# Kernel tuning notes

Measured on AMD Instinct MI355X. Metric: run time of the kernel, lower is better.

Reference implementation:

```python
import jax, jax.numpy as jnp
import numpy as np


def setup_inputs() -> dict:
    key = jax.random.key(0)
    k1, k2, k3 = jax.random.split(key, 3)
    B, L, D = 4, 2056, 1024  # L = K + T = 8 + 2048
    x = jax.random.normal(k1, (B, L, D), dtype=jnp.float32)
    # Linear weights stored as (in_features, out_features); no bias (config.bias=False)
    W_attn = jax.random.normal(k2, (D, 3 * D), dtype=jnp.float32) * 0.02
    W_proj = jax.random.normal(k3, (D, D), dtype=jnp.float32) * 0.02
    return {"x": x, "W_attn": W_attn, "W_proj": W_proj, "n_head": 16, "n_memory": 8}


def reference(x, W_attn, W_proj, n_head, n_memory):
    B, L, C = x.shape
    K = n_memory
    T = L - K
    hd = C // n_head
    scale = 1.0 / np.sqrt(hd).astype(np.float32)

    qkv = x @ W_attn                      # (B, L, 3C)
    q, k, v = jnp.split(qkv, 3, axis=2)
    # (B, H, L, hd)
    q = q.reshape(B, L, n_head, hd).transpose(0, 2, 1, 3)
    k = k.reshape(B, L, n_head, hd).transpose(0, 2, 1, 3)
    v = v.reshape(B, L, n_head, hd).transpose(0, 2, 1, 3)

    att = jnp.einsum("bhqd,bhkd->bhqk", q, k) * scale  # (B, H, L, L)

    # Mask: all-True except the (seq x seq) block which is causal (lower-tri).
    # Memory rows (first K) attend everywhere; seq rows attend to all memory + causal seq.
    mask = jnp.ones((L, L), dtype=bool)
    seq_causal = jnp.tril(jnp.ones((T, T), dtype=bool))
    mask = mask.at[K:, K:].set(seq_causal)

    att = jnp.where(mask[None, None, :, :], att, jnp.float32(-jnp.inf))
    att = jax.nn.softmax(att, axis=-1)

    y = jnp.einsum("bhqk,bhkd->bhqd", att, v)  # (B, H, L, hd)
    y = y.transpose(0, 2, 1, 3).reshape(B, L, C)
    return y @ W_proj
```

## Files before the change

### kernel.cpp

```cpp
#include <hip/hip_runtime.h>
#include <hip/hip_bf16.h>
#include <hip/hip_fp16.h>

typedef _Float16 f16x8 __attribute__((ext_vector_type(8)));
typedef _Float16 f16x4 __attribute__((ext_vector_type(4)));
typedef float f32x4 __attribute__((ext_vector_type(4)));

typedef const __attribute__((address_space(1))) void gvoid_t;
typedef __attribute__((address_space(3))) void svoid_t;

constexpr int Bb = 4, Lq = 2056, Dd = 1024, NH = 16, HD = 64, NMEM = 8;
constexpr int Mtot = Bb * Lq;
constexpr int KEYS = 64;
constexpr int NT = (Lq + KEYS - 1) / KEYS;
constexpr int NTQP = 17;
constexpr int LqV = 2064;

__device__ inline float fexp2(float x) {
  float r;
  asm("v_exp_f32 %0, %1" : "=v"(r) : "v"(x));
  return r;
}

__global__ __launch_bounds__(256) void cast_f16(const float* __restrict__ in,
                                                _Float16* __restrict__ out, int n8) {
  int i = blockIdx.x * blockDim.x + threadIdx.x;
  if (i >= n8) return;
  const float4* p = reinterpret_cast<const float4*>(in) + (size_t)i * 2;
  float4 a = p[0], b = p[1];
  f16x8 o;
  o[0] = (_Float16)a.x; o[1] = (_Float16)a.y; o[2] = (_Float16)a.z; o[3] = (_Float16)a.w;
  o[4] = (_Float16)b.x; o[5] = (_Float16)b.y; o[6] = (_Float16)b.z; o[7] = (_Float16)b.w;
  *(reinterpret_cast<f16x8*>(out) + i) = o;
}

__global__ void transpose_cast(const float* __restrict__ in, _Float16* __restrict__ out,
                               int rows, int cols) {
  __shared__ float t[32][33];
  int c0 = blockIdx.x * 32, r0 = blockIdx.y * 32;
  int tx = threadIdx.x, ty = threadIdx.y;
#pragma unroll
  for (int i = 0; i < 4; ++i)
    t[ty + i * 8][tx] = in[(size_t)(r0 + ty + i * 8) * cols + c0 + tx];
  __syncthreads();
#pragma unroll
  for (int i = 0; i < 4; ++i)
    out[(size_t)(c0 + ty + i * 8) * rows + r0 + tx] = (_Float16)t[tx][ty + i * 8];
}

template <int EPI>
__global__ __launch_bounds__(256) void gemm_f16(
    const _Float16* __restrict__ A, const _Float16* __restrict__ Bt,
    int M, int N, int Kd, float* __restrict__ Cf,
    _Float16* __restrict__ qout, _Float16* __restrict__ kout, _Float16* __restrict__ vtout) {
  constexpr int BM = 128, BN = 128, BK = 64;
  __shared__ _Float16 smem[2][2 * BM * BK];
  const int tid = threadIdx.x;
  const int wid = tid >> 6, lane = tid & 63;
  const int wr = wid >> 1, wc = wid & 1;
  const int l16 = lane & 15, lq = lane >> 4;

  const int gx = gridDim.x;
  const int nwg = gx * gridDim.y;
  const int i0 = blockIdx.y * gx + blockIdx.x;
  const int cpx = nwg >> 3;
  const int logical = (i0 & 7) * cpx + (i0 >> 3);
  const int m0 = (logical / gx) * BM, n0 = (logical % gx) * BN;

  f32x4 acc[4][4];
#pragma unroll
  for (int i = 0; i < 4; ++i)
#pragma unroll
    for (int j = 0; j < 4; ++j) acc[i][j] = (f32x4){0.f, 0.f, 0.f, 0.f};

  auto stage = [&](int sb, int kt) {
    const size_t kbase = (size_t)kt * BK;
    _Float16* sm = smem[sb];
#pragma unroll
    for (int c = 0; c < 4; ++c) {
      int q = wid * 256 + c * 64 + lane;
      int r = q >> 3, cc = q & 7;
      int gr = m0 + r; gr = gr < M ? gr : M - 1;
      const _Float16* src = A + (size_t)gr * Kd + kbase + ((cc ^ (r & 7)) << 3);
      __builtin_amdgcn_global_load_lds((gvoid_t*)src,
          (svoid_t*)(sm + (size_t)(wid * 256 + c * 64) * 8), 16, 0, 0);
    }
#pragma unroll
    for (int c = 0; c < 4; ++c) {
      int q = wid * 256 + c * 64 + lane;
      int r = q >> 3, cc = q & 7;
      const _Float16* src = Bt + (size_t)(n0 + r) * Kd + kbase + ((cc ^ (r & 7)) << 3);
      __builtin_amdgcn_global_load_lds((gvoid_t*)src,
          (svoid_t*)(sm + BM * BK + (size_t)(wid * 256 + c * 64) * 8), 16, 0, 0);
    }
  };

  const int KT = Kd / BK;
  stage(0, 0);
  __syncthreads();
  int sbuf = 0;
  for (int kt = 0; kt < KT; ++kt) {
    if (kt + 1 < KT) stage(sbuf ^ 1, kt + 1);
    const _Float16* sm = smem[sbuf];
#pragma unroll
    for (int kk = 0; kk < 2; ++kk) {
      f16x8 af[4], bfr[4];
#pragma unroll
      for (int i = 0; i < 4; ++i) {
        int r = wr * 64 + i * 16 + l16;
        int off = r * 64 + (((kk * 4 + lq) ^ (r & 7)) << 3);
        af[i] = *(const f16x8*)(sm + off);
      }
#pragma unroll
      for (int j = 0; j < 4; ++j) {
        int r = wc * 64 + j * 16 + l16;
        int off = BM * BK + r * 64 + (((kk * 4 + lq) ^ (r & 7)) << 3);
        bfr[j] = *(const f16x8*)(sm + off);
      }
#pragma unroll
      for (int i = 0; i < 4; ++i)
#pragma unroll
        for (int j = 0; j < 4; ++j)
          acc[i][j] = __builtin_amdgcn_mfma_f32_16x16x32_f16(af[i], bfr[j], acc[i][j], 0, 0, 0);
    }
    __syncthreads();
    sbuf ^= 1;
  }

  if (EPI == 1 && n0 >= 2 * Dd) {
#pragma unroll
    for (int i = 0; i < 4; ++i) {
      int mb = m0 + wr * 64 + i * 16 + lq * 4;
      if (mb >= M) continue;
      int b = mb / Lq, l = mb - b * Lq;
#pragma unroll
      for (int j = 0; j < 4; ++j) {
        int n = n0 + wc * 64 + j * 16 + l16;
        int h = (n >> 6) & 15, d = n & 63;
        if (l + 4 <= Lq) {
          int kk = l & 63;
          int ks = kk >> 5, rem = kk & 31, half = rem >> 4, idx = rem & 15;
          int col = (l & ~63) + (ks * 4 + (idx >> 2)) * 8 + half * 4;
          f16x4 pk;
          pk[0] = (_Float16)acc[i][j][0]; pk[1] = (_Float16)acc[i][j][1];
          pk[2] = (_Float16)acc[i][j][2]; pk[3] = (_Float16)acc[i][j][3];
          *(f16x4*)(vtout + ((size_t)(b * NH + h) * HD + d) * LqV + col) = pk;
        } else {
#pragma unroll
          for (int r = 0; r < 4; ++r) {
            int m = mb + r;
            if (m >= M) continue;
            int b2 = m / Lq, l2 = m - b2 * Lq;
            int kk = l2 & 63;
            int ks = kk >> 5, rem = kk & 31, half = rem >> 4, idx = rem & 15;
            int col = (l2 & ~63) + (ks * 4 + (idx >> 2)) * 8 + half * 4 + (idx & 3);
            vtout[((size_t)(b2 * NH + h) * HD + d) * LqV + col] = (_Float16)acc[i][j][r];
          }
        }
      }
    }
  } else {
#pragma unroll
    for (int i = 0; i < 4; ++i) {
#pragma unroll
      for (int r = 0; r < 4; ++r) {
        int m = m0 + wr * 64 + i * 16 + lq * 4 + r;
        if (m >= M) continue;
        if (EPI == 0) {
#pragma unroll
          for (int j = 0; j < 4; ++j) {
            int n = n0 + wc * 64 + j * 16 + l16;
            Cf[(size_t)m * N + n] = acc[i][j][r];
          }
        } else {
          int b = m / Lq, l = m - b * Lq;
#pragma unroll
          for (int j = 0; j < 4; ++j) {
            int n = n0 + wc * 64 + j * 16 + l16;
            int which = n >> 10, h = (n >> 6) & 15, d = n & 63;
            int bh = b * NH + h;
            _Float16 v = (_Float16)acc[i][j][r];
            if (which == 0)
              qout[((size_t)bh * Lq + l) * HD + d] = v;
            else
              kout[((size_t)bh * Lq + l) * HD + d] = v;
          }
        }
      }
    }
  }
}

__global__ __launch_bounds__(256) void attn_f16(const _Float16* __restrict__ qm,
                                                const _Float16* __restrict__ km,
                                                const _Float16* __restrict__ vt,
                                                _Float16* __restrict__ y) {
  __shared__ _Float16 kls[2][KEYS * HD];
  __shared__ _Float16 vls[2][KEYS * HD];

  const int i0 = blockIdx.y * (int)gridDim.x + blockIdx.x;
  const int logical = (i0 & 7) * (NTQP * Bb * NH / 8) + (i0 >> 3);
  const int bh = logical / NTQP;
  const int px = logical % NTQP;

  const int wid = threadIdx.x >> 6, lane = threadIdx.x & 63;
  const int l16 = lane & 15, lq = lane >> 4;

  const _Float16* qbase = qm + (size_t)bh * Lq * HD;
  const _Float16* kbase = km + (size_t)bh * Lq * HD;
  const _Float16* vbase = vt + (size_t)bh * HD * LqV;
  const int b = bh >> 4, h = bh & 15;

  const _Float16 QSC = (_Float16)(0.125f * 1.44269504f);

  f16x8 ones;
#pragma unroll
  for (int e = 0; e < 8; ++e) ones[e] = (_Float16)1.0f;

  const int qA = (wid * 2 + 0) * 64 + lane, qB = (wid * 2 + 1) * 64 + lane;
  const int rA = qA >> 3, cA = qA & 7;
  const int rB = qB >> 3, cB = qB & 7;
  const int ofA = (cA ^ (rA & 7)) << 3;
  const int ofB = (cB ^ (rB & 7)) << 3;
  _Float16* dKA0 = &kls[0][(wid * 2 + 0) * 512]; _Float16* dKB0 = &kls[0][(wid * 2 + 1) * 512];
  _Float16* dKA1 = &kls[1][(wid * 2 + 0) * 512]; _Float16* dKB1 = &kls[1][(wid * 2 + 1) * 512];
  _Float16* dVA0 = &vls[0][(wid * 2 + 0) * 512]; _Float16* dVB0 = &vls[0][(wid * 2 + 1) * 512];
  _Float16* dVA1 = &vls[1][(wid * 2 + 0) * 512]; _Float16* dVB1 = &vls[1][(wid * 2 + 1) * 512];

  const int nseg = (px == 0) ? 1 : 2;
  for (int seg = 0; seg < nseg; ++seg) {
    const int qt = (px == 0) ? 0 : (seg == 0 ? NT - px : px);
    const int qr0 = qt * 64 + wid * 16;

    int qrow = qr0 + l16; if (qrow > Lq - 1) qrow = Lq - 1;
    f16x8 qf0 = *(const f16x8*)(qbase + (size_t)qrow * HD + lq * 8);
    f16x8 qf1 = *(const f16x8*)(qbase + (size_t)qrow * HD + 32 + lq * 8);
#pragma unroll
    for (int e = 0; e < 8; ++e) {
      qf0[e] *= QSC;
      qf1[e] *= QSC;
    }

    const int irow = qr0 + l16;
    const int kmax = (irow < NMEM) ? (Lq - 1) : (irow < Lq - 1 ? irow : Lq - 1);

    f32x4 o[4];
#pragma unroll
    for (int dt = 0; dt < 4; ++dt) o[dt] = (f32x4){0.f, 0.f, 0.f, 0.f};
    f32x4 ol = (f32x4){0.f, 0.f, 0.f, 0.f};

    const int ntiles = (qt == 0) ? NT : (qt + 1 < NT ? qt + 1 : NT);

    const _Float16* pkA = kbase + (size_t)rA * HD + ofA;
    const _Float16* pkB = kbase + (size_t)rB * HD + ofB;
    const _Float16* pvA = vbase + (size_t)rA * LqV + ofA;
    const _Float16* pvB = vbase + (size_t)rB * LqV + ofB;

    auto stage_fast = [&](_Float16* dK0, _Float16* dK1, _Float16* dV0, _Float16* dV1) {
      __builtin_amdgcn_global_load_lds((gvoid_t*)pkA, (svoid_t*)dK0, 16, 0, 0);
      __builtin_amdgcn_global_load_lds((gvoid_t*)pkB, (svoid_t*)dK1, 16, 0, 0);
      __builtin_amdgcn_global_load_lds((gvoid_t*)pvA, (svoid_t*)dV0, 16, 0, 0);
      __builtin_amdgcn_global_load_lds((gvoid_t*)pvB, (svoid_t*)dV1, 16, 0, 0);
      pkA += KEYS * HD; pkB += KEYS * HD; pvA += KEYS; pvB += KEYS;
    };
    auto stage_clamp = [&](_Float16* dK0, _Float16* dK1, _Float16* dV0, _Float16* dV1) {
      int keyA = 2048 + rA; if (keyA > Lq - 1) keyA = Lq - 1;
      int keyB = 2048 + rB; if (keyB > Lq - 1) keyB = Lq - 1;
      __builtin_amdgcn_global_load_lds((gvoid_t*)(kbase + (size_t)keyA * HD + ofA),
                                       (svoid_t*)dK0, 16, 0, 0);
      __builtin_amdgcn_global_load_lds((gvoid_t*)(kbase + (size_t)keyB * HD + ofB),
                                       (svoid_t*)dK1, 16, 0, 0);
      int kcA = 2048 + ofA; if (kcA + 8 > LqV) kcA = LqV - 8;
      int kcB = 2048 + ofB; if (kcB + 8 > LqV) kcB = LqV - 8;
      __builtin_amdgcn_global_load_lds((gvoid_t*)(vbase + (size_t)rA * LqV + kcA),
                                       (svoid_t*)dV0, 16, 0, 0);
      __builtin_amdgcn_global_load_lds((gvoid_t*)(vbase + (size_t)rB * LqV + kcB),
                                       (svoid_t*)dV1, 16, 0, 0);
    };

    auto compute = [&](const _Float16* Kl, const _Float16* Vl, int t) {
      const int j0 = t * KEYS;
      const bool fastw = ((t + 1) * KEYS <= qr0);
      const int lim = kmax - j0;
#pragma unroll
      for (int ks = 0; ks < 2; ++ks) {
        const int r0 = ks * 32 + l16, r1 = r0 + 16;
        f16x8 ka0 = *(const f16x8*)(Kl + r0 * 64 + ((lq ^ (r0 & 7)) << 3));
        f16x8 kb0 = *(const f16x8*)(Kl + r0 * 64 + (((4 + lq) ^ (r0 & 7)) << 3));
        f16x8 ka1 = *(const f16x8*)(Kl + r1 * 64 + ((lq ^ (r1 & 7)) << 3));
        f16x8 kb1 = *(const f16x8*)(Kl + r1 * 64 + (((4 + lq) ^ (r1 & 7)) << 3));
        f32x4 s0 = (f32x4){0.f, 0.f, 0.f, 0.f};
        f32x4 s1 = (f32x4){0.f, 0.f, 0.f, 0.f};
        __builtin_amdgcn_s_setprio(1);
        s0 = __builtin_amdgcn_mfma_f32_16x16x32_f16(ka0, qf0, s0, 0, 0, 0);
        s0 = __builtin_amdgcn_mfma_f32_16x16x32_f16(kb0, qf1, s0, 0, 0, 0);
        s1 = __builtin_amdgcn_mfma_f32_16x16x32_f16(ka1, qf0, s1, 0, 0, 0);
        s1 = __builtin_amdgcn_mfma_f32_16x16x32_f16(kb1, qf1, s1, 0, 0, 0);
        __builtin_amdgcn_s_setprio(0);

        f16x8 pf;
        if (fastw) {
#pragma unroll
          for (int r = 0; r < 4; ++r) {
            pf[r] = (_Float16)fexp2(s0[r]);
            pf[4 + r] = (_Float16)fexp2(s1[r]);
          }
        } else {
          const int kb = ks * 32 + lq * 4;
#pragma unroll
          for (int r = 0; r < 4; ++r) {
            pf[r] = (kb + r <= lim) ? (_Float16)fexp2(s0[r]) : (_Float16)0.f;
            pf[4 + r] = (kb + 16 + r <= lim) ? (_Float16)fexp2(s1[r]) : (_Float16)0.f;
          }
        }

        __builtin_amdgcn_s_setprio(1);
        ol = __builtin_amdgcn_mfma_f32_16x16x32_f16(pf, ones, ol, 0, 0, 0);
#pragma unroll
        for (int dt = 0; dt < 4; ++dt) {
          const int vr = dt * 16 + l16;
          const int g = ks * 4 + lq;
          f16x8 vf = *(const f16x8*)(Vl + vr * 64 + ((g ^ (vr & 7)) << 3));
          o[dt] = __builtin_amdgcn_mfma_f32_16x16x32_f16(pf, vf, o[dt], 0, 0, 0);
        }
        __builtin_amdgcn_s_setprio(0);
      }
    };

    stage_fast(dKA0, dKB0, dVA0, dVB0);
    __syncthreads();
    int t = 0;
    for (;;) {
      {
        int nxt = t + 1;
        if (nxt < ntiles) {
          if (nxt == NT - 1) stage_clamp(dKA1, dKB1, dVA1, dVB1);
          else stage_fast(dKA1, dKB1, dVA1, dVB1);
        }
      }
      compute(kls[0], vls[0], t);
      __syncthreads();
      if (++t >= ntiles) break;
      {
        int nxt = t + 1;
        if (nxt < ntiles) {
          if (nxt == NT - 1) stage_clamp(dKA0, dKB0, dVA0, dVB0);
          else stage_fast(dKA0, dKB0, dVA0, dVB0);
        }
      }
      compute(kls[1], vls[1], t);
      __syncthreads();
      if (++t >= ntiles) break;
    }

#pragma unroll
    for (int r = 0; r < 4; ++r) {
      int orow = qr0 + lq * 4 + r;
      if (orow >= Lq) continue;
      float inv = 1.0f / ol[r];
#pragma unroll
      for (int dt = 0; dt < 4; ++dt)
        y[((size_t)(b * Lq + orow)) * Dd + h * HD + dt * 16 + l16] = (_Float16)(o[dt][r] * inv);
    }
  }
}

extern "C" void kernel_launch(void* const* d_in, const int* in_sizes, int n_in,
                              void* d_out, int out_size, void* d_ws, size_t ws_size,
                              hipStream_t stream) {
  (void)in_sizes; (void)n_in; (void)out_size; (void)ws_size;
  const float* x = (const float*)d_in[0];
  const float* W_attn = (const float*)d_in[1];
  const float* W_proj = (const float*)d_in[2];
  float* out = (float*)d_out;

  char* w = (char*)d_ws;
  _Float16* xh  = (_Float16*)(w);
  _Float16* wta = (_Float16*)(w + 16842752);
  _Float16* wtp = (_Float16*)(w + 23134208);
  _Float16* qh  = (_Float16*)(w + 25231360);
  _Float16* kh  = (_Float16*)(w + 42074112);
  _Float16* vth = (_Float16*)(w + 58916864);
  _Float16* yh  = xh;

  cast_f16<<<dim3((Mtot * Dd) / 8 / 256), dim3(256), 0, stream>>>(x, xh, (Mtot * Dd) / 8);
  transpose_cast<<<dim3(3 * Dd / 32, Dd / 32), dim3(32, 8), 0, stream>>>(W_attn, wta, Dd, 3 * Dd);
  transpose_cast<<<dim3(Dd / 32, Dd / 32), dim3(32, 8), 0, stream>>>(W_proj, wtp, Dd, Dd);

  gemm_f16<1><<<dim3(3 * Dd / 128, (Mtot + 127) / 128), dim3(256), 0, stream>>>(
      xh, wta, Mtot, 3 * Dd, Dd, nullptr, qh, kh, vth);

  attn_f16<<<dim3(NTQP, Bb * NH), dim3(256), 0, stream>>>(qh, kh, vth, yh);

  gemm_f16<0><<<dim3(Dd / 128, (Mtot + 127) / 128), dim3(256), 0, stream>>>(
      yh, wtp, Mtot, Dd, Dd, out, nullptr, nullptr, nullptr);
}
```

Before: 204.7 us.

## Process both paired query tiles in one pass sharing staged K/V tiles

```diff
diff --git a/kernel.cpp b/kernel.cpp
--- a/kernel.cpp
+++ b/kernel.cpp
@@ -217,9 +217,41 @@
 #pragma unroll
   for (int e = 0; e < 8; ++e) ones[e] = (_Float16)1.0f;
 
-  const int qA = (wid * 2 + 0) * 64 + lane, qB = (wid * 2 + 1) * 64 + lane;
-  const int rA = qA >> 3, cA = qA & 7;
-  const int rB = qB >> 3, cB = qB & 7;
+  const int qtA = (px == 0) ? 0 : NT - px;
+  const int ntA = (px == 0) ? NT : (qtA + 1 < NT ? qtA + 1 : NT);
+  const int ntB = (px == 0) ? 0 : px + 1;
+  const int qr0A = qtA * 64 + wid * 16;
+  const int qr0B = px * 64 + wid * 16;
+
+  int qrowA = qr0A + l16; if (qrowA > Lq - 1) qrowA = Lq - 1;
+  f16x8 qfA0 = *(const f16x8*)(qbase + (size_t)qrowA * HD + lq * 8);
+  f16x8 qfA1 = *(const f16x8*)(qbase + (size_t)qrowA * HD + 32 + lq * 8);
+  int qrowB = qr0B + l16;
+  f16x8 qfB0 = *(const f16x8*)(qbase + (size_t)qrowB * HD + lq * 8);
+  f16x8 qfB1 = *(const f16x8*)(qbase + (size_t)qrowB * HD + 32 + lq * 8);
+#pragma unroll
+  for (int e = 0; e < 8; ++e) {
+    qfA0[e] *= QSC; qfA1[e] *= QSC;
+    qfB0[e] *= QSC; qfB1[e] *= QSC;
+  }
+
+  const int irowA = qr0A + l16;
+  const int kmaxA = (irowA < NMEM) ? (Lq - 1) : (irowA < Lq - 1 ? irowA : Lq - 1);
+  const int irowB = qr0B + l16;
+  const int kmaxB = (irowB < NMEM) ? (Lq - 1) : irowB;
+
+  f32x4 oA[4], oB[4];
+#pragma unroll
+  for (int dt = 0; dt < 4; ++dt) {
+    oA[dt] = (f32x4){0.f, 0.f, 0.f, 0.f};
+    oB[dt] = (f32x4){0.f, 0.f, 0.f, 0.f};
+  }
+  f32x4 olA = (f32x4){0.f, 0.f, 0.f, 0.f};
+  f32x4 olB = (f32x4){0.f, 0.f, 0.f, 0.f};
+
+  const int qA_ = (wid * 2 + 0) * 64 + lane, qB_ = (wid * 2 + 1) * 64 + lane;
+  const int rA = qA_ >> 3, cA = qA_ & 7;
+  const int rB = qB_ >> 3, cB = qB_ & 7;
   const int ofA = (cA ^ (rA & 7)) << 3;
   const int ofB = (cB ^ (rB & 7)) << 3;
   _Float16* dKA0 = &kls[0][(wid * 2 + 0) * 512]; _Float16* dKB0 = &kls[0][(wid * 2 + 1) * 512];
@@ -227,140 +259,154 @@
   _Float16* dVA0 = &vls[0][(wid * 2 + 0) * 512]; _Float16* dVB0 = &vls[0][(wid * 2 + 1) * 512];
   _Float16* dVA1 = &vls[1][(wid * 2 + 0) * 512]; _Float16* dVB1 = &vls[1][(wid * 2 + 1) * 512];
 
-  const int nseg = (px == 0) ? 1 : 2;
-  for (int seg = 0; seg < nseg; ++seg) {
-    const int qt = (px == 0) ? 0 : (seg == 0 ? NT - px : px);
-    const int qr0 = qt * 64 + wid * 16;
-
-    int qrow = qr0 + l16; if (qrow > Lq - 1) qrow = Lq - 1;
-    f16x8 qf0 = *(const f16x8*)(qbase + (size_t)qrow * HD + lq * 8);
-    f16x8 qf1 = *(const f16x8*)(qbase + (size_t)qrow * HD + 32 + lq * 8);
-#pragma unroll
-    for (int e = 0; e < 8; ++e) {
-      qf0[e] *= QSC;
-      qf1[e] *= QSC;
-    }
-
-    const int irow = qr0 + l16;
-    const int kmax = (irow < NMEM) ? (Lq - 1) : (irow < Lq - 1 ? irow : Lq - 1);
-
-    f32x4 o[4];
-#pragma unroll
-    for (int dt = 0; dt < 4; ++dt) o[dt] = (f32x4){0.f, 0.f, 0.f, 0.f};
-    f32x4 ol = (f32x4){0.f, 0.f, 0.f, 0.f};
-
-    const int ntiles = (qt == 0) ? NT : (qt + 1 < NT ? qt + 1 : NT);
-
-    const _Float16* pkA = kbase + (size_t)rA * HD + ofA;
-    const _Float16* pkB = kbase + (size_t)rB * HD + ofB;
-    const _Float16* pvA = vbase + (size_t)rA * LqV + ofA;
-    const _Float16* pvB = vbase + (size_t)rB * LqV + ofB;
-
-    auto stage_fast = [&](_Float16* dK0, _Float16* dK1, _Float16* dV0, _Float16* dV1) {
-      __builtin_amdgcn_global_load_lds((gvoid_t*)pkA, (svoid_t*)dK0, 16, 0, 0);
-      __builtin_amdgcn_global_load_lds((gvoid_t*)pkB, (svoid_t*)dK1, 16, 0, 0);
-      __builtin_amdgcn_global_load_lds((gvoid_t*)pvA, (svoid_t*)dV0, 16, 0, 0);
-      __builtin_amdgcn_global_load_lds((gvoid_t*)pvB, (svoid_t*)dV1, 16, 0, 0);
-      pkA += KEYS * HD; pkB += KEYS * HD; pvA += KEYS; pvB += KEYS;
-    };
-    auto stage_clamp = [&](_Float16* dK0, _Float16* dK1, _Float16* dV0, _Float16* dV1) {
-      int keyA = 2048 + rA; if (keyA > Lq - 1) keyA = Lq - 1;
-      int keyB = 2048 + rB; if (keyB > Lq - 1) keyB = Lq - 1;
-      __builtin_amdgcn_global_load_lds((gvoid_t*)(kbase + (size_t)keyA * HD + ofA),
-                                       (svoid_t*)dK0, 16, 0, 0);
-      __builtin_amdgcn_global_load_lds((gvoid_t*)(kbase + (size_t)keyB * HD + ofB),
-                                       (svoid_t*)dK1, 16, 0, 0);
-      int kcA = 2048 + ofA; if (kcA + 8 > LqV) kcA = LqV - 8;
-      int kcB = 2048 + ofB; if (kcB + 8 > LqV) kcB = LqV - 8;
-      __builtin_amdgcn_global_load_lds((gvoid_t*)(vbase + (size_t)rA * LqV + kcA),
-                                       (svoid_t*)dV0, 16, 0, 0);
-      __builtin_amdgcn_global_load_lds((gvoid_t*)(vbase + (size_t)rB * LqV + kcB),
-                                       (svoid_t*)dV1, 16, 0, 0);
-    };
-
-    auto compute = [&](const _Float16* Kl, const _Float16* Vl, int t) {
-      const int j0 = t * KEYS;
-      const bool fastw = ((t + 1) * KEYS <= qr0);
-      const int lim = kmax - j0;
-#pragma unroll
-      for (int ks = 0; ks < 2; ++ks) {
-        const int r0 = ks * 32 + l16, r1 = r0 + 16;
-        f16x8 ka0 = *(const f16x8*)(Kl + r0 * 64 + ((lq ^ (r0 & 7)) << 3));
-        f16x8 kb0 = *(const f16x8*)(Kl + r0 * 64 + (((4 + lq) ^ (r0 & 7)) << 3));
-        f16x8 ka1 = *(const f16x8*)(Kl + r1 * 64 + ((lq ^ (r1 & 7)) << 3));
-        f16x8 kb1 = *(const f16x8*)(Kl + r1 * 64 + (((4 + lq) ^ (r1 & 7)) << 3));
-        f32x4 s0 = (f32x4){0.f, 0.f, 0.f, 0.f};
-        f32x4 s1 = (f32x4){0.f, 0.f, 0.f, 0.f};
-        __builtin_amdgcn_s_setprio(1);
-        s0 = __builtin_amdgcn_mfma_f32_16x16x32_f16(ka0, qf0, s0, 0, 0, 0);
-        s0 = __builtin_amdgcn_mfma_f32_16x16x32_f16(kb0, qf1, s0, 0, 0, 0);
-        s1 = __builtin_amdgcn_mfma_f32_16x16x32_f16(ka1, qf0, s1, 0, 0, 0);
-        s1 = __builtin_amdgcn_mfma_f32_16x16x32_f16(kb1, qf1, s1, 0, 0, 0);
-        __builtin_amdgcn_s_setprio(0);
-
-        f16x8 pf;
-        if (fastw) {
+  const _Float16* pkA = kbase + (size_t)rA * HD + ofA;
+  const _Float16* pkB = kbase + (size_t)rB * HD + ofB;
+  const _Float16* pvA = vbase + (size_t)rA * LqV + ofA;
+  const _Float16* pvB = vbase + (size_t)rB * LqV + ofB;
+
+  auto stage_fast = [&](_Float16* dK0, _Float16* dK1, _Float16* dV0, _Float16* dV1) {
+    __builtin_amdgcn_global_load_lds((gvoid_t*)pkA, (svoid_t*)dK0, 16, 0, 0);
+    __builtin_amdgcn_global_load_lds((gvoid_t*)pkB, (svoid_t*)dK1, 16, 0, 0);
+    __builtin_amdgcn_global_load_lds((gvoid_t*)pvA, (svoid_t*)dV0, 16, 0, 0);
+    __builtin_amdgcn_global_load_lds((gvoid_t*)pvB, (svoid_t*)dV1, 16, 0, 0);
+    pkA += KEYS * HD; pkB += KEYS * HD; pvA += KEYS; pvB += KEYS;
+  };
+  auto stage_clamp = [&](_Float16* dK0, _Float16* dK1, _Float16* dV0, _Float16* dV1) {
+    int keyA = 2048 + rA; if (keyA > Lq - 1) keyA = Lq - 1;
+    int keyB = 2048 + rB; if (keyB > Lq - 1) keyB = Lq - 1;
+    __builtin_amdgcn_global_load_lds((gvoid_t*)(kbase + (size_t)keyA * HD + ofA),
+                                     (svoid_t*)dK0, 16, 0, 0);
+    __builtin_amdgcn_global_load_lds((gvoid_t*)(kbase + (size_t)keyB * HD + ofB),
+                                     (svoid_t*)dK1, 16, 0, 0);
+    int kcA = 2048 + ofA; if (kcA + 8 > LqV) kcA = LqV - 8;
+    int kcB = 2048 + ofB; if (kcB + 8 > LqV) kcB = LqV - 8;
+    __builtin_amdgcn_global_load_lds((gvoid_t*)(vbase + (size_t)rA * LqV + kcA),
+                                     (svoid_t*)dV0, 16, 0, 0);
+    __builtin_amdgcn_global_load_lds((gvoid_t*)(vbase + (size_t)rB * LqV + kcB),
+                                     (svoid_t*)dV1, 16, 0, 0);
+  };
+
+  auto compute = [&](const _Float16* Kl, const _Float16* Vl, int t, bool dualB) {
+    const int j0 = t * KEYS;
+    const bool fastA = ((t + 1) * KEYS <= qr0A);
+    const bool fastB = ((t + 1) * KEYS <= qr0B);
+    const int limA = kmaxA - j0, limB = kmaxB - j0;
+#pragma unroll
+    for (int ks = 0; ks < 2; ++ks) {
+      const int r0 = ks * 32 + l16, r1 = r0 + 16;
+      f16x8 ka0 = *(const f16x8*)(Kl + r0 * 64 + ((lq ^ (r0 & 7)) << 3));
+      f16x8 kb0 = *(const f16x8*)(Kl + r0 * 64 + (((4 + lq) ^ (r0 & 7)) << 3));
+      f16x8 ka1 = *(const f16x8*)(Kl + r1 * 64 + ((lq ^ (r1 & 7)) << 3));
+      f16x8 kb1 = *(const f16x8*)(Kl + r1 * 64 + (((4 + lq) ^ (r1 & 7)) << 3));
+      f32x4 sA0 = (f32x4){0.f, 0.f, 0.f, 0.f};
+      f32x4 sA1 = (f32x4){0.f, 0.f, 0.f, 0.f};
+      f32x4 sB0 = (f32x4){0.f, 0.f, 0.f, 0.f};
+      f32x4 sB1 = (f32x4){0.f, 0.f, 0.f, 0.f};
+      __builtin_amdgcn_s_setprio(1);
+      sA0 = __builtin_amdgcn_mfma_f32_16x16x32_f16(ka0, qfA0, sA0, 0, 0, 0);
+      sA0 = __builtin_amdgcn_mfma_f32_16x16x32_f16(kb0, qfA1, sA0, 0, 0, 0);
+      sA1 = __builtin_amdgcn_mfma_f32_16x16x32_f16(ka1, qfA0, sA1, 0, 0, 0);
+      sA1 = __builtin_amdgcn_mfma_f32_16x16x32_f16(kb1, qfA1, sA1, 0, 0, 0);
+      if (dualB) {
+        sB0 = __builtin_amdgcn_mfma_f32_16x16x32_f16(ka0, qfB0, sB0, 0, 0, 0);
+        sB0 = __builtin_amdgcn_mfma_f32_16x16x32_f16(kb0, qfB1, sB0, 0, 0, 0);
+        sB1 = __builtin_amdgcn_mfma_f32_16x16x32_f16(ka1, qfB0, sB1, 0, 0, 0);
+        sB1 = __builtin_amdgcn_mfma_f32_16x16x32_f16(kb1, qfB1, sB1, 0, 0, 0);
+      }
+      __builtin_amdgcn_s_setprio(0);
+
+      const int kb = ks * 32 + lq * 4;
+      f16x8 pfA, pfB;
+      if (fastA) {
+#pragma unroll
+        for (int r = 0; r < 4; ++r) {
+          pfA[r] = (_Float16)fexp2(sA0[r]);
+          pfA[4 + r] = (_Float16)fexp2(sA1[r]);
+        }
+      } else {
+#pragma unroll
+        for (int r = 0; r < 4; ++r) {
+          pfA[r] = (kb + r <= limA) ? (_Float16)fexp2(sA0[r]) : (_Float16)0.f;
+          pfA[4 + r] = (kb + 16 + r <= limA) ? (_Float16)fexp2(sA1[r]) : (_Float16)0.f;
+        }
+      }
+      if (dualB) {
+        if (fastB) {
 #pragma unroll
           for (int r = 0; r < 4; ++r) {
-            pf[r] = (_Float16)fexp2(s0[r]);
-            pf[4 + r] = (_Float16)fexp2(s1[r]);
+            pfB[r] = (_Float16)fexp2(sB0[r]);
+            pfB[4 + r] = (_Float16)fexp2(sB1[r]);
           }
         } else {
-          const int kb = ks * 32 + lq * 4;
 #pragma unroll
           for (int r = 0; r < 4; ++r) {
-            pf[r] = (kb + r <= lim) ? (_Float16)fexp2(s0[r]) : (_Float16)0.f;
-            pf[4 + r] = (kb + 16 + r <= lim) ? (_Float16)fexp2(s1[r]) : (_Float16)0.f;
+            pfB[r] = (kb + r <= limB) ? (_Float16)fexp2(sB0[r]) : (_Float16)0.f;
+            pfB[4 + r] = (kb + 16 + r <= limB) ? (_Float16)fexp2(sB1[r]) : (_Float16)0.f;
           }
         }
-
-        __builtin_amdgcn_s_setprio(1);
-        ol = __builtin_amdgcn_mfma_f32_16x16x32_f16(pf, ones, ol, 0, 0, 0);
-#pragma unroll
-        for (int dt = 0; dt < 4; ++dt) {
-          const int vr = dt * 16 + l16;
-          const int g = ks * 4 + lq;
-          f16x8 vf = *(const f16x8*)(Vl + vr * 64 + ((g ^ (vr & 7)) << 3));
-          o[dt] = __builtin_amdgcn_mfma_f32_16x16x32_f16(pf, vf, o[dt], 0, 0, 0);
-        }
-        __builtin_amdgcn_s_setprio(0);
-      }
-    };
-
-    stage_fast(dKA0, dKB0, dVA0, dVB0);
+      }
+
+      __builtin_amdgcn_s_setprio(1);
+      olA = __builtin_amdgcn_mfma_f32_16x16x32_f16(pfA, ones, olA, 0, 0, 0);
+      if (dualB) olB = __builtin_amdgcn_mfma_f32_16x16x32_f16(pfB, ones, olB, 0, 0, 0);
+#pragma unroll
+      for (int dt = 0; dt < 4; ++dt) {
+        const int vr = dt * 16 + l16;
+        const int g = ks * 4 + lq;
+        f16x8 vf = *(const f16x8*)(Vl + vr * 64 + ((g ^ (vr & 7)) << 3));
+        oA[dt] = __builtin_amdgcn_mfma_f32_16x16x32_f16(pfA, vf, oA[dt], 0, 0, 0);
+        if (dualB) oB[dt] = __builtin_amdgcn_mfma_f32_16x16x32_f16(pfB, vf, oB[dt], 0, 0, 0);
+      }
+      __builtin_amdgcn_s_setprio(0);
+    }
+  };
+
+  stage_fast(dKA0, dKB0, dVA0, dVB0);
+  __syncthreads();
+  int t = 0;
+  for (;;) {
+    {
+      int nxt = t + 1;
+      if (nxt < ntA) {
+        if (nxt == NT - 1) stage_clamp(dKA1, dKB1, dVA1, dVB1);
+        else stage_fast(dKA1, dKB1, dVA1, dVB1);
+      }
+    }
+    compute(kls[0], vls[0], t, t < ntB);
     __syncthreads();
-    int t = 0;
-    for (;;) {
-      {
-        int nxt = t + 1;
-        if (nxt < ntiles) {
-          if (nxt == NT - 1) stage_clamp(dKA1, dKB1, dVA1, dVB1);
-          else stage_fast(dKA1, dKB1, dVA1, dVB1);
-        }
-      }
-      compute(kls[0], vls[0], t);
-      __syncthreads();
-      if (++t >= ntiles) break;
-      {
-        int nxt = t + 1;
-        if (nxt < ntiles) {
-          if (nxt == NT - 1) stage_clamp(dKA0, dKB0, dVA0, dVB0);
-          else stage_fast(dKA0, dKB0, dVA0, dVB0);
-        }
-      }
-      compute(kls[1], vls[1], t);
-      __syncthreads();
-      if (++t >= ntiles) break;
-    }
-
+    if (++t >= ntA) break;
+    {
+      int nxt = t + 1;
+      if (nxt < ntA) {
+        if (nxt == NT - 1) stage_clamp(dKA0, dKB0, dVA0, dVB0);
+        else stage_fast(dKA0, dKB0, dVA0, dVB0);
+      }
+    }
+    compute(kls[1], vls[1], t, t < ntB);
+    __syncthreads();
+    if (++t >= ntA) break;
+  }
+
+#pragma unroll
+  for (int r = 0; r < 4; ++r) {
+    int orowA = qr0A + lq * 4 + r;
+    if (orowA < Lq) {
+      float inv = 1.0f / olA[r];
+#pragma unroll
+      for (int dt = 0; dt < 4; ++dt)
+        y[((size_t)(b * Lq + orowA)) * Dd + h * HD + dt * 16 + l16] =
+            (_Float16)(oA[dt][r] * inv);
+    }
+  }
+  if (px > 0) {
 #pragma unroll
     for (int r = 0; r < 4; ++r) {
-      int orow = qr0 + lq * 4 + r;
-      if (orow >= Lq) continue;
-      float inv = 1.0f / ol[r];
+      int orowB = qr0B + lq * 4 + r;
+      float inv = 1.0f / olB[r];
 #pragma unroll
       for (int dt = 0; dt < 4; ++dt)
-        y[((size_t)(b * Lq + orow)) * Dd + h * HD + dt * 16 + l16] = (_Float16)(o[dt][r] * inv);
+        y[((size_t)(b * Lq + orowB)) * Dd + h * HD + dt * 16 + l16] =
+            (_Float16)(oB[dt][r] * inv);
     }
   }
 }
```

Measured after the change: 212.3 us. 3.7% more time.
